# Optimization experiments

Hardware: AMD Instinct MI355X
Metric: run time of the kernel (lower is better)

## Reference

```python
import jax, jax.numpy as jnp
import numpy as np

B, S, H = 1, 2048, 2048
NH, NOPE, ROPE, VHD = 16, 128, 64, 128
QHD = NOPE + ROPE            # 192
QLR, KVLR, FF = 1536, 512, 8192
SCALE = QHD ** -0.5          # rope_scaling is None -> mscale = 1
EPS = 1e-6
THETA = 10000.0


def _rms(x, w):
    return x * jax.lax.rsqrt(jnp.mean(x * x, axis=-1, keepdims=True) + EPS) * w


def _rotate_half(x):
    x1, x2 = x[..., : x.shape[-1] // 2], x[..., x.shape[-1] // 2 :]
    return jnp.concatenate((-x2, x1), axis=-1)


def _rope(x, cos, sin, pos):
    # x: (b, h, s, d). First de-interleave pairs: (even dims | odd dims),
    # matching the reshape/transpose in apply_rotary_pos_emb.
    b, h, s, d = x.shape
    x = x.reshape(b, h, s, d // 2, 2).transpose(0, 1, 2, 4, 3).reshape(b, h, s, d)
    c = cos[pos][:, None]   # (b, 1, s, d)
    sn = sin[pos][:, None]
    return x * c + _rotate_half(x) * sn


def setup_inputs() -> dict:
    key = jax.random.key(0)
    ks = jax.random.split(key, 10)
    w = lambda k, shp: jax.random.normal(k, shp, jnp.float32) * 0.02
    hidden_states = jax.random.normal(ks[0], (B, S, H), jnp.float32)
    position_ids = jnp.tile(jnp.arange(S, dtype=jnp.int32)[None], (B, 1))
    inv_freq = 1.0 / (THETA ** (jnp.arange(0, ROPE, 2, dtype=jnp.float32) / ROPE))
    freqs = jnp.arange(S, dtype=jnp.float32)[:, None] * inv_freq[None, :]
    emb = jnp.concatenate([freqs, freqs], axis=-1)  # (S, ROPE)
    return {
        "hidden_states": hidden_states,
        "sin": jnp.sin(emb),
        "cos": jnp.cos(emb),
        "wq_a": w(ks[1], (H, QLR)),
        "q_a_ln": jnp.ones((QLR,), jnp.float32),
        "wq_b": w(ks[2], (QLR, NH * QHD)),
        "wkv_a": w(ks[3], (H, KVLR + ROPE)),
        "kv_a_ln": jnp.ones((KVLR,), jnp.float32),
        "wkv_b": w(ks[4], (KVLR, NH * (NOPE + VHD))),
        "wo": w(ks[5], (NH * VHD, H)),
        "in_ln": jnp.ones((H,), jnp.float32),
        "post_ln": jnp.ones((H,), jnp.float32),
        "w_gate": w(ks[6], (H, FF)),
        "w_up": w(ks[7], (H, FF)),
        "w_down": w(ks[8], (FF, H)),
        "position_ids": position_ids,
    }


def reference(hidden_states, sin, cos, wq_a, q_a_ln, wq_b, wkv_a, kv_a_ln,
              wkv_b, wo, in_ln, post_ln, w_gate, w_up, w_down, position_ids):
    residual = hidden_states
    x = _rms(hidden_states, in_ln)

    # --- MLA: low-rank Q ---
    q = _rms(x @ wq_a, q_a_ln) @ wq_b                       # (B,S,NH*QHD)
    q = q.reshape(B, S, NH, QHD).transpose(0, 2, 1, 3)      # (B,NH,S,QHD)
    q_nope, q_pe = q[..., :NOPE], q[..., NOPE:]

    # --- low-rank KV with shared (MQA) rope key ---
    ckv = x @ wkv_a                                          # (B,S,KVLR+ROPE)
    k_pe = ckv[..., KVLR:].reshape(B, S, 1, ROPE).transpose(0, 2, 1, 3)
    kv = (_rms(ckv[..., :KVLR], kv_a_ln) @ wkv_b)
    kv = kv.reshape(B, S, NH, NOPE + VHD).transpose(0, 2, 1, 3)
    k_nope, v = kv[..., :NOPE], kv[..., NOPE:]

    q_pe = _rope(q_pe, cos, sin, position_ids)
    k_pe = _rope(k_pe, cos, sin, position_ids)

    qs = jnp.concatenate([q_nope, q_pe], axis=-1)            # (B,NH,S,QHD)
    ks = jnp.concatenate([k_nope, jnp.broadcast_to(k_pe, (B, NH, S, ROPE))], axis=-1)

    scores = jnp.einsum("bhqd,bhkd->bhqk", qs, ks) * SCALE
    causal = jnp.tril(jnp.ones((S, S), bool))
    scores = jnp.where(causal, scores, jnp.finfo(scores.dtype).min)
    attn = jax.nn.softmax(scores, axis=-1)
    out = jnp.einsum("bhqk,bhkd->bhqd", attn, v)
    out = out.transpose(0, 2, 1, 3).reshape(B, S, NH * VHD)
    hidden = residual + out @ wo

    # --- dense gated-SiLU MLP ---
    residual = hidden
    y = _rms(hidden, post_ln)
    mlp = (jax.nn.silu(y @ w_gate) * (y @ w_up)) @ w_down
    return residual + mlp
```

## Files before the change

### kernel.cpp

```cpp
#include <hip/hip_runtime.h>
#include <math.h>

#define ATTN_SCALE 0.07216878364870322f

typedef __attribute__((ext_vector_type(8))) short short8;
typedef __attribute__((ext_vector_type(4))) float floatx4;

__device__ __forceinline__ unsigned short f2bf(float f) {
    union { float f; unsigned int u; } v; v.f = f;
    unsigned int r = v.u + 0x7fffu + ((v.u >> 16) & 1u);
    return (unsigned short)(r >> 16);
}
__device__ __forceinline__ float bf2f(unsigned short h) {
    union { unsigned int u; float f; } v; v.u = ((unsigned int)h) << 16;
    return v.f;
}
__device__ __forceinline__ void gld16(const void* g, void* l) {
    __builtin_amdgcn_global_load_lds(
        (const __attribute__((address_space(1))) unsigned int*)g,
        (__attribute__((address_space(3))) unsigned int*)l, 16, 0, 0);
}

__global__ __launch_bounds__(256) void rms_kernel(
    const float* __restrict__ in, int ld_in,
    const float* __restrict__ w,
    unsigned short* __restrict__ out, int ld_out, int N)
{
    const int row = blockIdx.x;
    const int tid = threadIdx.x;
    const float* x = in + (size_t)row * ld_in;
    float ss = 0.f;
    for (int i = tid * 4; i < N; i += 1024) {
        float4 v = *(const float4*)(x + i);
        ss += v.x * v.x + v.y * v.y + v.z * v.z + v.w * v.w;
    }
    #pragma unroll
    for (int off = 32; off > 0; off >>= 1)
        ss += __shfl_down(ss, off);
    __shared__ float red[4];
    const int lane = tid & 63, wid = tid >> 6;
    if (lane == 0) red[wid] = ss;
    __syncthreads();
    const float tot = red[0] + red[1] + red[2] + red[3];
    const float rs = rsqrtf(tot / (float)N + 1e-6f);
    unsigned short* o = out + (size_t)row * ld_out;
    for (int i = tid * 4; i < N; i += 1024) {
        float4 v = *(const float4*)(x + i);
        float4 wv = *(const float4*)(w + i);
        __align__(8) unsigned short ov[4];
        ov[0] = f2bf(v.x * rs * wv.x);
        ov[1] = f2bf(v.y * rs * wv.y);
        ov[2] = f2bf(v.z * rs * wv.z);
        ov[3] = f2bf(v.w * rs * wv.w);
        *(uint2*)&o[i] = *(uint2*)ov;
    }
}

__global__ __launch_bounds__(256) void cast_transpose_kernel(
    const float* __restrict__ W, unsigned short* __restrict__ Wt,
    int K, int N)
{
    __shared__ float tile[64][65];
    const int tid = threadIdx.x;
    const int kb = blockIdx.y * 64;
    const int nb = blockIdx.x * 64;
    const int r  = tid >> 2;
    const int c0 = (tid & 3) * 16;
    if (nb + 64 <= N) {
        #pragma unroll
        for (int j = 0; j < 16; j += 4)
            *(float4*)&tile[r][c0 + j] =
                *(const float4*)&W[(size_t)(kb + r) * N + nb + c0 + j];
    } else {
        for (int j = 0; j < 16; ++j) {
            int n = nb + c0 + j;
            tile[r][c0 + j] = (n < N) ? W[(size_t)(kb + r) * N + n] : 0.f;
        }
    }
    __syncthreads();
    __align__(16) unsigned short ov[16];
    #pragma unroll
    for (int j = 0; j < 16; ++j) ov[j] = f2bf(tile[c0 + j][r]);
    int4* dst = (int4*)&Wt[(size_t)(nb + r) * K + kb + c0];
    dst[0] = ((int4*)ov)[0];
    dst[1] = ((int4*)ov)[1];
}

__global__ __launch_bounds__(256) void gemm_bf16_kernel(
    const unsigned short* __restrict__ A,
    const unsigned short* __restrict__ Bt,
    float* __restrict__ C,
    unsigned short* __restrict__ Cb,
    const float* __restrict__ R,
    int N, int K)
{
    __shared__ __align__(16) unsigned short As[2][4096];
    __shared__ __align__(16) unsigned short Bs[2][4096];
    const int tid = threadIdx.x;
    const int w  = tid >> 6;
    const int l  = tid & 63;
    const int lm = l & 15;
    const int lk = l >> 4;
    const int row0 = blockIdx.y * 128;
    const int col0 = blockIdx.x * 128;
    const int wm = (w >> 1) * 64;
    const int wn = (w & 1) * 64;
    const int nsplit = gridDim.z;
    const int kz = blockIdx.z;
    const int kchunk = K / nsplit;
    const int kbase = kz * kchunk;

    const unsigned short* a0 = A  + (size_t)(row0 + w * 16 + lm) * K + kbase + lk * 8;
    const unsigned short* a1 = a0 + (size_t)64 * K;
    const unsigned short* b0 = Bt + (size_t)(col0 + w * 16 + lm) * K + kbase + lk * 8;
    const unsigned short* b1 = b0 + (size_t)64 * K;
    const int s0 = w * 512 + l * 8;
    const int s1 = (w + 4) * 512 + l * 8;

    floatx4 acc[4][4];
    #pragma unroll
    for (int i = 0; i < 4; ++i)
        #pragma unroll
        for (int j = 0; j < 4; ++j)
            acc[i][j] = (floatx4){0.f, 0.f, 0.f, 0.f};

    gld16(a0, &As[0][s0]);
    gld16(a1, &As[0][s1]);
    gld16(b0, &Bs[0][s0]);
    gld16(b1, &Bs[0][s1]);
    a0 += 32; a1 += 32; b0 += 32; b1 += 32;
    __syncthreads();

    const int niter = kchunk >> 5;
    int cur = 0;
    for (int t = 0; t < niter; ++t) {
        if (t + 1 < niter) {
            gld16(a0, &As[cur ^ 1][s0]);
            gld16(a1, &As[cur ^ 1][s1]);
            gld16(b0, &Bs[cur ^ 1][s0]);
            gld16(b1, &Bs[cur ^ 1][s1]);
            a0 += 32; a1 += 32; b0 += 32; b1 += 32;
        }
        short8 af[4], bg_[4];
        #pragma unroll
        for (int i = 0; i < 4; ++i)
            af[i] = *(const short8*)&As[cur][((w >> 1) * 4 + i) * 512 + l * 8];
        #pragma unroll
        for (int j = 0; j < 4; ++j)
            bg_[j] = *(const short8*)&Bs[cur][((w & 1) * 4 + j) * 512 + l * 8];
        #pragma unroll
        for (int i = 0; i < 4; ++i)
            #pragma unroll
            for (int j = 0; j < 4; ++j)
                acc[i][j] = __builtin_amdgcn_mfma_f32_16x16x32_bf16(
                    af[i], bg_[j], acc[i][j], 0, 0, 0);
        __syncthreads();
        cur ^= 1;
    }

    const int quad = l >> 4;
    const bool ng = (col0 + 128 > N);
    #pragma unroll
    for (int i = 0; i < 4; ++i) {
        #pragma unroll
        for (int r = 0; r < 4; ++r) {
            const int m = row0 + wm + i * 16 + quad * 4 + r;
            #pragma unroll
            for (int j = 0; j < 4; ++j) {
                const int n = col0 + wn + j * 16 + lm;
                if (ng && n >= N) continue;
                const size_t off = (size_t)m * N + n;
                float v = acc[i][j][r];
                if (nsplit > 1) {
                    if (R && kz == 0) v += R[off];
                    unsafeAtomicAdd(&C[off], v);
                } else if (Cb) {
                    Cb[off] = f2bf(v);
                } else {
                    if (R) v += R[off];
                    C[off] = v;
                }
            }
        }
    }
}

__global__ __launch_bounds__(512) void gemm256_kernel(
    const unsigned short* __restrict__ A,
    const unsigned short* __restrict__ Bt,
    float* __restrict__ C,
    unsigned short* __restrict__ Cb,
    const float* __restrict__ R,
    int N, int K)
{
    __shared__ __align__(16) unsigned short As[2][16384];
    __shared__ __align__(16) unsigned short Bs[2][16384];
    const int tid = threadIdx.x;
    const int w   = tid >> 6;
    const int l   = tid & 63;
    const int lm  = l & 15;
    const int quad = l >> 4;
    const int wm2 = w >> 2;
    const int wn4 = w & 3;

    const int gx = gridDim.x;
    const int nwg = gx * gridDim.y;
    int bid = blockIdx.y * gx + blockIdx.x;
    {
        const int q = nwg >> 3, r = nwg & 7;
        const int xcd = bid & 7, off = bid >> 3;
        bid = (xcd < r ? xcd * (q + 1) : r * (q + 1) + (xcd - r) * q) + off;
    }
    const int row0 = (bid / gx) * 256;
    const int col0 = (bid % gx) * 256;

    const int nsplit = gridDim.z;
    const int kz = blockIdx.z;
    const int kchunk = K / nsplit;
    const int kbase = kz * kchunk;

    const int slk = (tid >> 4) & 7;
    const int srg = tid >> 7;
    const unsigned short* sa = A  + (size_t)(row0 + srg * 16 + lm) * K + kbase + slk * 8;
    const unsigned short* sb = Bt + (size_t)(col0 + srg * 16 + lm) * K + kbase + slk * 8;

    floatx4 acc[8][4];
    #pragma unroll
    for (int i = 0; i < 8; ++i)
        #pragma unroll
        for (int j = 0; j < 4; ++j)
            acc[i][j] = (floatx4){0.f, 0.f, 0.f, 0.f};

    const int nt = kchunk >> 6;
    #pragma unroll
    for (int j = 0; j < 4; ++j) {
        gld16(sa + (size_t)j * 64 * K, (char*)As[0] + j * 8192 + tid * 16);
        gld16(sb + (size_t)j * 64 * K, (char*)Bs[0] + j * 8192 + tid * 16);
    }
    asm volatile("s_waitcnt vmcnt(0)" ::: "memory");
    __builtin_amdgcn_sched_barrier(0);
    __builtin_amdgcn_s_barrier();
    __builtin_amdgcn_sched_barrier(0);

    for (int t = 0; t < nt; ++t) {
        const int p = t & 1;
        const char* ab = (const char*)As[p] + wm2 * 16384 + l * 16;
        const char* bb = (const char*)Bs[p] + wn4 * 8192  + l * 16;
        char* dA = (char*)As[p ^ 1] + tid * 16;
        char* dB = (char*)Bs[p ^ 1] + tid * 16;
        const size_t ko = (size_t)(t + 1) * 64;
        const bool pre = (t + 1 < nt);
        short8 bfr[4][2];
        short8 afr[2][2];

        #pragma unroll
        for (int q = 0; q < 4; ++q) {
            if (q == 0) {
                #pragma unroll
                for (int j = 0; j < 4; ++j) {
                    bfr[j][0] = *(const short8*)(bb + j * 2048);
                    bfr[j][1] = *(const short8*)(bb + j * 2048 + 1024);
                }
            }
            afr[0][0] = *(const short8*)(ab + (2 * q) * 2048);
            afr[0][1] = *(const short8*)(ab + (2 * q) * 2048 + 1024);
            afr[1][0] = *(const short8*)(ab + (2 * q + 1) * 2048);
            afr[1][1] = *(const short8*)(ab + (2 * q + 1) * 2048 + 1024);
            if (pre) {
                if (q == 0) {
                    gld16(sa + ko, dA);
                    gld16(sb + ko, dB);
                    gld16(sa + (size_t)64 * K + ko, dA + 8192);
                    gld16(sb + (size_t)64 * K + ko, dB + 8192);
                } else if (q == 1) {
                    gld16(sa + (size_t)128 * K + ko, dA + 16384);
                    gld16(sb + (size_t)128 * K + ko, dB + 16384);
                    gld16(sa + (size_t)192 * K + ko, dA + 24576);
                    gld16(sb + (size_t)192 * K + ko, dB + 24576);
                }
            }
            __builtin_amdgcn_sched_barrier(0);
            __builtin_amdgcn_s_barrier();
            __builtin_amdgcn_sched_barrier(0);
            __builtin_amdgcn_s_setprio(1);
            #pragma unroll
            for (int c = 0; c < 2; ++c)
                #pragma unroll
                for (int i2 = 0; i2 < 2; ++i2)
                    #pragma unroll
                    for (int j = 0; j < 4; ++j)
                        acc[2 * q + i2][j] = __builtin_amdgcn_mfma_f32_16x16x32_bf16(
                            afr[i2][c], bfr[j][c], acc[2 * q + i2][j], 0, 0, 0);
            __builtin_amdgcn_s_setprio(0);
            __builtin_amdgcn_sched_barrier(0);
            if (q == 3)
                asm volatile("s_waitcnt vmcnt(0)" ::: "memory");
            __builtin_amdgcn_s_barrier();
            __builtin_amdgcn_sched_barrier(0);
        }
    }

    #pragma unroll
    for (int i = 0; i < 8; ++i) {
        #pragma unroll
        for (int r = 0; r < 4; ++r) {
            const int m = row0 + wm2 * 128 + i * 16 + quad * 4 + r;
            #pragma unroll
            for (int j = 0; j < 4; ++j) {
                const int n = col0 + wn4 * 64 + j * 16 + lm;
                const size_t off = (size_t)m * N + n;
                float v = acc[i][j][r];
                if (nsplit > 1) {
                    if (R && kz == 0) v += R[off];
                    unsafeAtomicAdd(&C[off], v);
                } else if (Cb) {
                    Cb[off] = f2bf(v);
                } else {
                    if (R) v += R[off];
                    C[off] = v;
                }
            }
        }
    }
}

__global__ __launch_bounds__(256) void rope_q_kernel(
    unsigned short* __restrict__ x,
    const float* __restrict__ cosb, const float* __restrict__ sinb,
    const int* __restrict__ pos_ids)
{
    const int gid = blockIdx.x * 256 + threadIdx.x;
    const int i = gid & 31;
    const int grp = gid >> 5;
    const int hh = grp & 15;
    const int row = grp >> 4;
    unsigned short* base = x + (size_t)row * 3072 + hh * 192 + 128;
    const float x0 = bf2f(base[2 * i]);
    const float x1 = bf2f(base[2 * i + 1]);
    const int p = pos_ids[row];
    const float c = cosb[p * 64 + i];
    const float s = sinb[p * 64 + i];
    __syncthreads();
    base[i]      = f2bf(x0 * c - x1 * s);
    base[32 + i] = f2bf(x1 * c + x0 * s);
}

__global__ __launch_bounds__(256) void rope_kpe_kernel(
    const float* __restrict__ ckv, unsigned short* __restrict__ kpe,
    const float* __restrict__ cosb, const float* __restrict__ sinb,
    const int* __restrict__ pos_ids)
{
    const int gid = blockIdx.x * 256 + threadIdx.x;
    const int i = gid & 31;
    const int row = gid >> 5;
    const float x0 = ckv[(size_t)row * 576 + 512 + 2 * i];
    const float x1 = ckv[(size_t)row * 576 + 512 + 2 * i + 1];
    const int p = pos_ids[row];
    const float c = cosb[p * 64 + i];
    const float s = sinb[p * 64 + i];
    kpe[(size_t)row * 64 + i]      = f2bf(x0 * c - x1 * s);
    kpe[(size_t)row * 64 + 32 + i] = f2bf(x1 * c + x0 * s);
}

__global__ __launch_bounds__(256) void vtrans_kernel(
    const unsigned short* __restrict__ kvb, unsigned short* __restrict__ vtg)
{
    __shared__ unsigned short tile[64][72];
    const int tid = threadIdx.x;
    const int s0 = blockIdx.x * 64;
    const int d0 = blockIdx.y * 64;
    const int h  = blockIdx.z;
    const int r  = tid >> 2;
    const int c0 = (tid & 3) * 16;
    *(int4*)&tile[r][c0] =
        *(const int4*)&kvb[(size_t)(s0 + r) * 4096 + h * 256 + 128 + d0 + c0];
    *(int4*)&tile[r][c0 + 8] =
        *(const int4*)&kvb[(size_t)(s0 + r) * 4096 + h * 256 + 128 + d0 + c0 + 8];
    __syncthreads();
    __align__(16) unsigned short ov[16];
    #pragma unroll
    for (int j = 0; j < 16; ++j) ov[j] = tile[c0 + j][r];
    unsigned short* dst = vtg + ((size_t)(h * 128 + d0 + r)) * 2048 + s0 + c0;
    ((int4*)dst)[0] = ((int4*)ov)[0];
    ((int4*)dst)[1] = ((int4*)ov)[1];
}

__global__ __launch_bounds__(512) void attn_mfma_kernel(
    const unsigned short* __restrict__ qb,
    const unsigned short* __restrict__ kvb,
    const unsigned short* __restrict__ kpe,
    const unsigned short* __restrict__ vtg,
    unsigned short* __restrict__ out)
{
    __shared__ __align__(16) unsigned short Kf[128 * 200];
    __shared__ __align__(16) unsigned short Vt[2][128 * 136];
    __shared__ __align__(16) unsigned short Ps[64 * 136];
    __shared__ float pmax_s[8][64];
    __shared__ float psum_s[8][64];
    __shared__ __align__(16) float m_state[64];
    __shared__ __align__(16) float l_state[64];
    __shared__ __align__(16) float alpha_s[64];
    __shared__ __align__(16) float mnew_s[64];

    const int tid  = threadIdx.x;
    const int w    = tid >> 6;
    const int l    = tid & 63;
    const int l15  = l & 15;
    const int quad = l >> 4;
    const int h    = blockIdx.y;
    const int qs   = (w & 3) * 16;
    const int dh   = (w >> 2) * 64;

    for (int pass = 0; pass < 2; ++pass) {
        const int qt = pass ? (31 - (int)blockIdx.x) : (int)blockIdx.x;
        const int q0 = qt * 64;
        const int ntiles = (qt >> 1) + 1;

        short8 qf[4][6];
        #pragma unroll
        for (int nt = 0; nt < 4; ++nt)
            #pragma unroll
            for (int c = 0; c < 6; ++c)
                qf[nt][c] = *(const short8*)&qb[(size_t)(q0 + nt * 16 + l15) * 3072
                                               + h * 192 + c * 32 + quad * 8];

        floatx4 oacc[4];
        #pragma unroll
        for (int nt = 0; nt < 4; ++nt) oacc[nt] = (floatx4){0.f, 0.f, 0.f, 0.f};
        if (tid < 64) { m_state[tid] = -3e38f; l_state[tid] = 0.f; }

        {
            const int k0 = 0;
            for (int s = w; s < 50; s += 8) {
                unsigned ab = s * 1024 + l * 16;
                unsigned row = ab / 400u;
                unsigned g = (ab - row * 400u) >> 4;
                const unsigned short* src;
                if (g < 16u)      src = kvb + (size_t)(k0 + row) * 4096 + h * 256 + g * 8;
                else if (g < 24u) src = kpe + (size_t)(k0 + row) * 64 + (g - 16u) * 8;
                else              src = kpe + (size_t)(k0 + row) * 64;
                gld16(src, (char*)Kf + ab);
            }
            for (int s = w; s < 34; s += 8) {
                unsigned ab = s * 1024 + l * 16;
                unsigned row = ab / 272u;
                unsigned g = (ab - row * 272u) >> 4;
                const unsigned short* src =
                    vtg + (size_t)(h * 128 + row) * 2048 + k0 + (g < 16u ? g * 8 : 0u);
                gld16(src, (char*)Vt[0] + ab);
            }
        }

        for (int kt = 0; kt < ntiles; ++kt) {
            const int k0 = kt * 128;
            const int vb = kt & 1;
            __syncthreads();

            floatx4 st[4];
            #pragma unroll
            for (int nt = 0; nt < 4; ++nt) st[nt] = (floatx4){0.f, 0.f, 0.f, 0.f};
            #pragma unroll
            for (int c = 0; c < 6; ++c) {
                short8 kf = *(const short8*)&Kf[(w * 16 + l15) * 200 + c * 32 + quad * 8];
                #pragma unroll
                for (int nt = 0; nt < 4; ++nt)
                    st[nt] = __builtin_amdgcn_mfma_f32_16x16x32_bf16(kf, qf[nt][c], st[nt], 0, 0, 0);
            }
            #pragma unroll
            for (int nt = 0; nt < 4; ++nt) {
                const int qq = q0 + nt * 16 + l15;
                float vmax = -3e38f;
                #pragma unroll
                for (int r = 0; r < 4; ++r) {
                    const int kpos = k0 + w * 16 + quad * 4 + r;
                    float v = st[nt][r] * ATTN_SCALE;
                    if (kpos > qq) v = -3e38f;
                    st[nt][r] = v;
                    vmax = fmaxf(vmax, v);
                }
                vmax = fmaxf(vmax, __shfl_xor(vmax, 16));
                vmax = fmaxf(vmax, __shfl_xor(vmax, 32));
                if (quad == 0) pmax_s[w][nt * 16 + l15] = vmax;
            }
            __syncthreads();
            if (tid < 64) {
                float mp = m_state[tid];
                float mn = mp;
                #pragma unroll
                for (int ww = 0; ww < 8; ++ww) mn = fmaxf(mn, pmax_s[ww][tid]);
                alpha_s[tid] = __expf(mp - mn);
                mnew_s[tid] = mn;
                m_state[tid] = mn;
            }
            __syncthreads();

            #pragma unroll
            for (int nt = 0; nt < 4; ++nt) {
                const float mn = mnew_s[nt * 16 + l15];
                float vsum = 0.f;
                __align__(8) unsigned short pb[4];
                #pragma unroll
                for (int r = 0; r < 4; ++r) {
                    float p = __expf(st[nt][r] - mn);
                    vsum += p;
                    pb[r] = f2bf(p);
                }
                *(uint2*)&Ps[(nt * 16 + l15) * 136 + w * 16 + quad * 4] = *(uint2*)pb;
                vsum += __shfl_xor(vsum, 16);
                vsum += __shfl_xor(vsum, 32);
                if (quad == 0) psum_s[w][nt * 16 + l15] = vsum;
            }
            {
                float4 al4 = *(const float4*)&alpha_s[qs + quad * 4];
                #pragma unroll
                for (int nt = 0; nt < 4; ++nt) {
                    oacc[nt][0] *= al4.x; oacc[nt][1] *= al4.y;
                    oacc[nt][2] *= al4.z; oacc[nt][3] *= al4.w;
                }
            }
            __syncthreads();
            if (tid < 64) {
                float acc = 0.f;
                #pragma unroll
                for (int ww = 0; ww < 8; ++ww) acc += psum_s[ww][tid];
                l_state[tid] = l_state[tid] * alpha_s[tid] + acc;
            }
            if (kt + 1 < ntiles) {
                const int k1 = k0 + 128;
                for (int s = w; s < 50; s += 8) {
                    unsigned ab = s * 1024 + l * 16;
                    unsigned row = ab / 400u;
                    unsigned g = (ab - row * 400u) >> 4;
                    const unsigned short* src;
                    if (g < 16u)      src = kvb + (size_t)(k1 + row) * 4096 + h * 256 + g * 8;
                    else if (g < 24u) src = kpe + (size_t)(k1 + row) * 64 + (g - 16u) * 8;
                    else              src = kpe + (size_t)(k1 + row) * 64;
                    gld16(src, (char*)Kf + ab);
                }
                for (int s = w; s < 34; s += 8) {
                    unsigned ab = s * 1024 + l * 16;
                    unsigned row = ab / 272u;
                    unsigned g = (ab - row * 272u) >> 4;
                    const unsigned short* src =
                        vtg + (size_t)(h * 128 + row) * 2048 + k1 + (g < 16u ? g * 8 : 0u);
                    gld16(src, (char*)Vt[vb ^ 1] + ab);
                }
            }
            #pragma unroll
            for (int c = 0; c < 4; ++c) {
                short8 pf = *(const short8*)&Ps[(qs + l15) * 136 + c * 32 + quad * 8];
                #pragma unroll
                for (int nt = 0; nt < 4; ++nt) {
                    short8 vf = *(const short8*)&Vt[vb][(dh + nt * 16 + l15) * 136
                                                       + c * 32 + quad * 8];
                    oacc[nt] = __builtin_amdgcn_mfma_f32_16x16x32_bf16(pf, vf, oacc[nt], 0, 0, 0);
                }
            }
        }
        __syncthreads();

        {
            float4 l4 = *(const float4*)&l_state[qs + quad * 4];
            float inv0 = 1.f / l4.x, inv1 = 1.f / l4.y, inv2 = 1.f / l4.z, inv3 = 1.f / l4.w;
            #pragma unroll
            for (int nt = 0; nt < 4; ++nt) {
                const size_t col = h * 128 + dh + nt * 16 + l15;
                out[(size_t)(q0 + qs + quad * 4 + 0) * 2048 + col] = f2bf(oacc[nt][0] * inv0);
                out[(size_t)(q0 + qs + quad * 4 + 1) * 2048 + col] = f2bf(oacc[nt][1] * inv1);
                out[(size_t)(q0 + qs + quad * 4 + 2) * 2048 + col] = f2bf(oacc[nt][2] * inv2);
                out[(size_t)(q0 + qs + quad * 4 + 3) * 2048 + col] = f2bf(oacc[nt][3] * inv3);
            }
        }
        __syncthreads();
    }
}

__global__ __launch_bounds__(256) void silu_mul_kernel(
    unsigned short* __restrict__ g, const unsigned short* __restrict__ u, int n8)
{
    int i = blockIdx.x * 256 + threadIdx.x;
    if (i >= n8) return;
    int4 gv = ((const int4*)g)[i];
    int4 uv = ((const int4*)u)[i];
    const unsigned short* gs = (const unsigned short*)&gv;
    const unsigned short* us = (const unsigned short*)&uv;
    __align__(16) unsigned short ov[8];
    #pragma unroll
    for (int j = 0; j < 8; ++j) {
        float gf = bf2f(gs[j]), uf = bf2f(us[j]);
        ov[j] = f2bf(gf * uf / (1.f + __expf(-gf)));
    }
    ((int4*)g)[i] = *(int4*)ov;
}

extern "C" void kernel_launch(void* const* d_in, const int* in_sizes, int n_in,
                              void* d_out, int out_size, void* d_ws, size_t ws_size,
                              hipStream_t stream)
{
    (void)in_sizes; (void)n_in; (void)out_size; (void)ws_size;
    const float* hidden  = (const float*)d_in[0];
    const float* sinb    = (const float*)d_in[1];
    const float* cosb    = (const float*)d_in[2];
    const float* wq_a    = (const float*)d_in[3];
    const float* q_a_ln  = (const float*)d_in[4];
    const float* wq_b    = (const float*)d_in[5];
    const float* wkv_a   = (const float*)d_in[6];
    const float* kv_a_ln = (const float*)d_in[7];
    const float* wkv_b   = (const float*)d_in[8];
    const float* wo      = (const float*)d_in[9];
    const float* in_ln   = (const float*)d_in[10];
    const float* post_ln = (const float*)d_in[11];
    const float* w_gate  = (const float*)d_in[12];
    const float* w_up    = (const float*)d_in[13];
    const float* w_down  = (const float*)d_in[14];
    const int*   pos     = (const int*)d_in[15];

    char* wsb = (char*)d_ws;
    size_t used = 0;
    auto alloc = [&](size_t bytes) {
        char* p = wsb + used;
        used += (bytes + 255) & ~(size_t)255;
        return p;
    };
    float* q_a   = (float*)alloc((size_t)2048 * 1536 * 4);
    float* ckv   = (float*)alloc((size_t)2048 * 576 * 4);
    float* h2    = (float*)alloc((size_t)2048 * 2048 * 4);
    unsigned short* xnb  = (unsigned short*)alloc((size_t)2048 * 2048 * 2);
    unsigned short* qab  = (unsigned short*)alloc((size_t)2048 * 1536 * 2);
    unsigned short* kvnb = (unsigned short*)alloc((size_t)2048 * 512 * 2);
    unsigned short* qbb  = (unsigned short*)alloc((size_t)2048 * 3072 * 2);
    unsigned short* kvbb = (unsigned short*)alloc((size_t)2048 * 4096 * 2);
    unsigned short* kpe  = (unsigned short*)alloc((size_t)2048 * 64 * 2);
    unsigned short* vtg  = (unsigned short*)alloc((size_t)16 * 128 * 2048 * 2);
    unsigned short* attb = (unsigned short*)alloc((size_t)2048 * 2048 * 2);
    unsigned short* gb   = (unsigned short*)alloc((size_t)2048 * 8192 * 2);
    unsigned short* ub   = (unsigned short*)alloc((size_t)2048 * 8192 * 2);
    unsigned short* wt   = (unsigned short*)alloc((size_t)16777216 * 2);
    float* outp = (float*)d_out;

    hipMemsetAsync(q_a, 0, (size_t)2048 * 1536 * 4, stream);
    hipMemsetAsync(ckv, 0, (size_t)2048 * 576 * 4, stream);
    hipMemsetAsync(h2, 0, (size_t)2048 * 2048 * 4, stream);
    hipMemsetAsync(outp, 0, (size_t)2048 * 2048 * 4, stream);

    rms_kernel<<<2048, 256, 0, stream>>>(hidden, 2048, in_ln, xnb, 2048, 2048);
    cast_transpose_kernel<<<dim3(24, 32), 256, 0, stream>>>(wq_a, wt, 2048, 1536);
    gemm_bf16_kernel<<<dim3(12, 16, 2), 256, 0, stream>>>(xnb, wt, q_a, nullptr, nullptr, 1536, 2048);
    rms_kernel<<<2048, 256, 0, stream>>>(q_a, 1536, q_a_ln, qab, 1536, 1536);
    cast_transpose_kernel<<<dim3(48, 24), 256, 0, stream>>>(wq_b, wt, 1536, 3072);
    gemm_bf16_kernel<<<dim3(24, 16), 256, 0, stream>>>(qab, wt, nullptr, qbb, nullptr, 3072, 1536);
    cast_transpose_kernel<<<dim3(10, 32), 256, 0, stream>>>(wkv_a, wt, 2048, 576);
    gemm_bf16_kernel<<<dim3(5, 16, 4), 256, 0, stream>>>(xnb, wt, ckv, nullptr, nullptr, 576, 2048);
    rms_kernel<<<2048, 256, 0, stream>>>(ckv, 576, kv_a_ln, kvnb, 512, 512);
    cast_transpose_kernel<<<dim3(64, 8), 256, 0, stream>>>(wkv_b, wt, 512, 4096);
    gemm_bf16_kernel<<<dim3(32, 16), 256, 0, stream>>>(kvnb, wt, nullptr, kvbb, nullptr, 4096, 512);
    rope_q_kernel<<<4096, 256, 0, stream>>>(qbb, cosb, sinb, pos);
    rope_kpe_kernel<<<256, 256, 0, stream>>>(ckv, kpe, cosb, sinb, pos);
    vtrans_kernel<<<dim3(32, 2, 16), 256, 0, stream>>>(kvbb, vtg);
    attn_mfma_kernel<<<dim3(16, 16), 512, 0, stream>>>(qbb, kvbb, kpe, vtg, attb);
    cast_transpose_kernel<<<dim3(32, 32), 256, 0, stream>>>(wo, wt, 2048, 2048);
    gemm256_kernel<<<dim3(8, 8, 4), 512, 0, stream>>>(attb, wt, h2, nullptr, hidden, 2048, 2048);
    rms_kernel<<<2048, 256, 0, stream>>>(h2, 2048, post_ln, xnb, 2048, 2048);
    cast_transpose_kernel<<<dim3(128, 32), 256, 0, stream>>>(w_gate, wt, 2048, 8192);
    gemm256_kernel<<<dim3(32, 8, 1), 512, 0, stream>>>(xnb, wt, nullptr, gb, nullptr, 8192, 2048);
    cast_transpose_kernel<<<dim3(128, 32), 256, 0, stream>>>(w_up, wt, 2048, 8192);
    gemm256_kernel<<<dim3(32, 8, 1), 512, 0, stream>>>(xnb, wt, nullptr, ub, nullptr, 8192, 2048);
    silu_mul_kernel<<<8192, 256, 0, stream>>>(gb, ub, 2097152);
    cast_transpose_kernel<<<dim3(32, 128), 256, 0, stream>>>(w_down, wt, 8192, 2048);
    gemm256_kernel<<<dim3(8, 8, 4), 512, 0, stream>>>(gb, wt, outp, nullptr, h2, 2048, 8192);
}
```

Baseline: 1.070 ms.

## Replace split-K atomic accumulation with partial buffers and a separate reduce kernel

Split-K GEMMs now write each K-slice's partial result with plain stores into scratch buffers (reusing the gb/ub/qbb allocations) instead of doing atomic adds into a zeroed output. A new float4 reduce kernel sums the partials and adds the residual. This lets the four hipMemsetAsync calls be removed. The cost is extra partial-buffer write and read traffic and four extra launches. The final GEMM's second partial pair overruns the qbb allocation into the following buffers, which are no longer live at that point.

```diff
diff --git a/kernel.cpp b/kernel.cpp
--- a/kernel.cpp
+++ b/kernel.cpp
@@ -86,12 +86,37 @@
     dst[1] = ((int4*)ov)[1];
 }
 
+__global__ __launch_bounds__(256) void reduce_kernel(
+    const float* __restrict__ p0, const float* __restrict__ p1,
+    const float* __restrict__ p2, const float* __restrict__ p3,
+    const float* __restrict__ R, float* __restrict__ out, int n4)
+{
+    int i = blockIdx.x * 256 + threadIdx.x;
+    if (i >= n4) return;
+    float4 a = ((const float4*)p0)[i];
+    float4 b = ((const float4*)p1)[i];
+    float4 s;
+    s.x = a.x + b.x; s.y = a.y + b.y; s.z = a.z + b.z; s.w = a.w + b.w;
+    if (p2) {
+        float4 c = ((const float4*)p2)[i];
+        float4 d = ((const float4*)p3)[i];
+        s.x += c.x + d.x; s.y += c.y + d.y; s.z += c.z + d.z; s.w += c.w + d.w;
+    }
+    if (R) {
+        float4 r = ((const float4*)R)[i];
+        s.x += r.x; s.y += r.y; s.z += r.z; s.w += r.w;
+    }
+    ((float4*)out)[i] = s;
+}
+
 __global__ __launch_bounds__(256) void gemm_bf16_kernel(
     const unsigned short* __restrict__ A,
     const unsigned short* __restrict__ Bt,
     float* __restrict__ C,
     unsigned short* __restrict__ Cb,
     const float* __restrict__ R,
+    float* __restrict__ P01,
+    float* __restrict__ P23,
     int N, int K)
 {
     __shared__ __align__(16) unsigned short As[2][4096];
@@ -160,6 +185,11 @@
 
     const int quad = l >> 4;
     const bool ng = (col0 + 128 > N);
+    float* P = nullptr;
+    if (P01) {
+        const size_t MN = (size_t)gridDim.y * 128 * N;
+        P = (kz < 2) ? (P01 + (size_t)kz * MN) : (P23 + (size_t)(kz - 2) * MN);
+    }
     #pragma unroll
     for (int i = 0; i < 4; ++i) {
         #pragma unroll
@@ -171,9 +201,8 @@
                 if (ng && n >= N) continue;
                 const size_t off = (size_t)m * N + n;
                 float v = acc[i][j][r];
-                if (nsplit > 1) {
-                    if (R && kz == 0) v += R[off];
-                    unsafeAtomicAdd(&C[off], v);
+                if (P) {
+                    P[off] = v;
                 } else if (Cb) {
                     Cb[off] = f2bf(v);
                 } else {
@@ -191,6 +220,8 @@
     float* __restrict__ C,
     unsigned short* __restrict__ Cb,
     const float* __restrict__ R,
+    float* __restrict__ P01,
+    float* __restrict__ P23,
     int N, int K)
 {
     __shared__ __align__(16) unsigned short As[2][16384];
@@ -300,6 +331,11 @@
         }
     }
 
+    float* P = nullptr;
+    if (P01) {
+        const size_t MN = (size_t)gridDim.y * 256 * N;
+        P = (kz < 2) ? (P01 + (size_t)kz * MN) : (P23 + (size_t)(kz - 2) * MN);
+    }
     #pragma unroll
     for (int i = 0; i < 8; ++i) {
         #pragma unroll
@@ -310,9 +346,8 @@
                 const int n = col0 + wn4 * 64 + j * 16 + lm;
                 const size_t off = (size_t)m * N + n;
                 float v = acc[i][j][r];
-                if (nsplit > 1) {
-                    if (R && kz == 0) v += R[off];
-                    unsafeAtomicAdd(&C[off], v);
+                if (P) {
+                    P[off] = v;
                 } else if (Cb) {
                     Cb[off] = f2bf(v);
                 } else {
@@ -638,34 +673,62 @@
     unsigned short* wt   = (unsigned short*)alloc((size_t)16777216 * 2);
     float* outp = (float*)d_out;
 
-    hipMemsetAsync(q_a, 0, (size_t)2048 * 1536 * 4, stream);
-    hipMemsetAsync(ckv, 0, (size_t)2048 * 576 * 4, stream);
-    hipMemsetAsync(h2, 0, (size_t)2048 * 2048 * 4, stream);
-    hipMemsetAsync(outp, 0, (size_t)2048 * 2048 * 4, stream);
-
     rms_kernel<<<2048, 256, 0, stream>>>(hidden, 2048, in_ln, xnb, 2048, 2048);
     cast_transpose_kernel<<<dim3(24, 32), 256, 0, stream>>>(wq_a, wt, 2048, 1536);
-    gemm_bf16_kernel<<<dim3(12, 16, 2), 256, 0, stream>>>(xnb, wt, q_a, nullptr, nullptr, 1536, 2048);
+    {
+        float* P = (float*)gb;
+        gemm_bf16_kernel<<<dim3(12, 16, 2), 256, 0, stream>>>(
+            xnb, wt, nullptr, nullptr, nullptr, P, P, 1536, 2048);
+        reduce_kernel<<<3072, 256, 0, stream>>>(
+            P, P + (size_t)2048 * 1536, nullptr, nullptr, nullptr, q_a, 786432);
+    }
     rms_kernel<<<2048, 256, 0, stream>>>(q_a, 1536, q_a_ln, qab, 1536, 1536);
     cast_transpose_kernel<<<dim3(48, 24), 256, 0, stream>>>(wq_b, wt, 1536, 3072);
-    gemm_bf16_kernel<<<dim3(24, 16), 256, 0, stream>>>(qab, wt, nullptr, qbb, nullptr, 3072, 1536);
+    gemm_bf16_kernel<<<dim3(24, 16), 256, 0, stream>>>(
+        qab, wt, nullptr, qbb, nullptr, nullptr, nullptr, 3072, 1536);
     cast_transpose_kernel<<<dim3(10, 32), 256, 0, stream>>>(wkv_a, wt, 2048, 576);
-    gemm_bf16_kernel<<<dim3(5, 16, 4), 256, 0, stream>>>(xnb, wt, ckv, nullptr, nullptr, 576, 2048);
+    {
+        float* P = (float*)ub;
+        const size_t MN = (size_t)2048 * 576;
+        gemm_bf16_kernel<<<dim3(5, 16, 4), 256, 0, stream>>>(
+            xnb, wt, nullptr, nullptr, nullptr, P, P + 2 * MN, 576, 2048);
+        reduce_kernel<<<1152, 256, 0, stream>>>(
+            P, P + MN, P + 2 * MN, P + 3 * MN, nullptr, ckv, 294912);
+    }
     rms_kernel<<<2048, 256, 0, stream>>>(ckv, 576, kv_a_ln, kvnb, 512, 512);
     cast_transpose_kernel<<<dim3(64, 8), 256, 0, stream>>>(wkv_b, wt, 512, 4096);
-    gemm_bf16_kernel<<<dim3(32, 16), 256, 0, stream>>>(kvnb, wt, nullptr, kvbb, nullptr, 4096, 512);
+    gemm_bf16_kernel<<<dim3(32, 16), 256, 0, stream>>>(
+        kvnb, wt, nullptr, kvbb, nullptr, nullptr, nullptr, 4096, 512);
     rope_q_kernel<<<4096, 256, 0, stream>>>(qbb, cosb, sinb, pos);
     rope_kpe_kernel<<<256, 256, 0, stream>>>(ckv, kpe, cosb, sinb, pos);
     vtrans_kernel<<<dim3(32, 2, 16), 256, 0, stream>>>(kvbb, vtg);
     attn_mfma_kernel<<<dim3(16, 16), 512, 0, stream>>>(qbb, kvbb, kpe, vtg, attb);
     cast_transpose_kernel<<<dim3(32, 32), 256, 0, stream>>>(wo, wt, 2048, 2048);
-    gemm256_kernel<<<dim3(8, 8, 4), 512, 0, stream>>>(attb, wt, h2, nullptr, hidden, 2048, 2048);
+    {
+        float* Pg = (float*)gb;
+        float* Pu = (float*)ub;
+        const size_t MN = (size_t)2048 * 2048;
+        gemm256_kernel<<<dim3(8, 8, 4), 512, 0, stream>>>(
+            attb, wt, nullptr, nullptr, nullptr, Pg, Pu, 2048, 2048);
+        reduce_kernel<<<4096, 256, 0, stream>>>(
+            Pg, Pg + MN, Pu, Pu + MN, hidden, h2, 1048576);
+    }
     rms_kernel<<<2048, 256, 0, stream>>>(h2, 2048, post_ln, xnb, 2048, 2048);
     cast_transpose_kernel<<<dim3(128, 32), 256, 0, stream>>>(w_gate, wt, 2048, 8192);
-    gemm256_kernel<<<dim3(32, 8, 1), 512, 0, stream>>>(xnb, wt, nullptr, gb, nullptr, 8192, 2048);
+    gemm256_kernel<<<dim3(32, 8, 1), 512, 0, stream>>>(
+        xnb, wt, nullptr, gb, nullptr, nullptr, nullptr, 8192, 2048);
     cast_transpose_kernel<<<dim3(128, 32), 256, 0, stream>>>(w_up, wt, 2048, 8192);
-    gemm256_kernel<<<dim3(32, 8, 1), 512, 0, stream>>>(xnb, wt, nullptr, ub, nullptr, 8192, 2048);
+    gemm256_kernel<<<dim3(32, 8, 1), 512, 0, stream>>>(
+        xnb, wt, nullptr, ub, nullptr, nullptr, nullptr, 8192, 2048);
     silu_mul_kernel<<<8192, 256, 0, stream>>>(gb, ub, 2097152);
     cast_transpose_kernel<<<dim3(32, 128), 256, 0, stream>>>(w_down, wt, 8192, 2048);
-    gemm256_kernel<<<dim3(8, 8, 4), 512, 0, stream>>>(gb, wt, outp, nullptr, h2, 2048, 8192);
-}
+    {
+        float* Pu = (float*)ub;
+        float* Pq = (float*)qbb;
+        const size_t MN = (size_t)2048 * 2048;
+        gemm256_kernel<<<dim3(8, 8, 4), 512, 0, stream>>>(
+            gb, wt, nullptr, nullptr, nullptr, Pu, Pq, 2048, 8192);
+        reduce_kernel<<<4096, 256, 0, stream>>>(
+            Pu, Pu + MN, Pq, Pq + MN, h2, outp, 1048576);
+    }
+}
```

Result: faster. 923.8 us (-13.7%).
